# Performance work log

Hardware: AMD Instinct MI355X
Metric: run time of the kernel (lower is better)

## Reference

```python
import jax, jax.numpy as jnp
import numpy as np

N_NODES = 100000
N_EDGES = 800000


def gcn_conv(x, W, b, src, dst, ew, n):
    # PyG GCNConv with edge weights and self-loops already included in (src, dst, ew):
    # deg[i] = sum of incoming edge weights at i; norm_e = d^-1/2[src] * w_e * d^-1/2[dst]
    h = x @ W                                                  # [N, F_out]
    deg = jax.ops.segment_sum(ew, dst, num_segments=n)         # [N]
    dinv = jnp.where(deg > 0, jax.lax.rsqrt(deg), 0.0)
    norm = dinv[src] * ew * dinv[dst]                          # [E]
    out = jax.ops.segment_sum(h[src] * norm[:, None], dst, num_segments=n)
    return out + b


def add_self_loops(edge_index, edge_weight, n):
    loop = jnp.arange(n, dtype=edge_index.dtype)
    src = jnp.concatenate([edge_index[0], loop])
    dst = jnp.concatenate([edge_index[1], loop])
    ew = jnp.concatenate([edge_weight, jnp.ones((n,), edge_weight.dtype)])
    return src, dst, ew


def setup_inputs() -> dict:
    key = jax.random.key(0)
    ks = jax.random.split(key, 10)
    x = jax.random.normal(ks[0], (N_NODES, 5), jnp.float32)
    edge_index = jax.random.randint(ks[1], (2, N_EDGES), 0, N_NODES, dtype=jnp.int64)
    edge_weight = jax.random.uniform(ks[2], (N_EDGES,), jnp.float32)
    def glorot(k, fan_in, fan_out):
        s = float(np.sqrt(6.0 / (fan_in + fan_out)))
        return jax.random.uniform(k, (fan_in, fan_out), jnp.float32, -s, s)
    return {
        "x": x,
        "edge_index": edge_index,
        "edge_weight": edge_weight,
        "W1": glorot(ks[3], 5, 320),
        "b1": jnp.zeros((320,), jnp.float32),
        "W2": glorot(ks[4], 320, 160),
        "b2": jnp.zeros((160,), jnp.float32),
        "We": glorot(ks[5], 160, 80),
        "be": jnp.zeros((80,), jnp.float32),
    }


def reference(x, edge_index, edge_weight, W1, b1, W2, b2, We, be):
    n = x.shape[0]
    src, dst, ew = add_self_loops(edge_index, edge_weight, n)
    h = gcn_conv(x, W1, b1, src, dst, ew, n)        # conv1
    h = jax.nn.relu(h)
    h = gcn_conv(h, W2, b2, src, dst, ew, n)        # conv2
    return h @ We + be                              # embed linear
```

## Files before the change

kernel.cpp:

```cpp
#include <hip/hip_runtime.h>

#define NF0 5
#define F1 320
#define F2 160
#define F3 80
#define NSUB 8
#define SUBCAP 512

typedef float f32x4 __attribute__((ext_vector_type(4)));
typedef _Float16 f16x8 __attribute__((ext_vector_type(8)));


__global__ void k_prep(int padz, int* __restrict__ zreg, int zwords,
                       const float* __restrict__ W2, const float* __restrict__ We,
                       _Float16* __restrict__ Bh,
                       const float* __restrict__ b2, const float* __restrict__ be,
                       float* __restrict__ bc,
                       const unsigned int* __restrict__ ei32, int E, int* __restrict__ flag) {
    __shared__ int ok;
    int b = blockIdx.x;
    if (b < padz) {
        int t = b * 256 + threadIdx.x;
        if (t < zwords) zreg[t] = 0;
        return;
    }
    b -= padz;
    if (b < 13) {
        int t = b * 256 + threadIdx.x;
        if (t >= 50 * 64) return;
        int fid = t >> 6, lane = t & 63;
        int kk = fid / 5, ct = fid % 5;
        int col = ct * 16 + (lane & 15);
        int row0 = kk * 32 + (lane >> 4) * 8;
        float acc[8] = {0.f, 0.f, 0.f, 0.f, 0.f, 0.f, 0.f, 0.f};
        for (int m = 0; m < F2; ++m) {
            float wv = We[m * F3 + col];
            #pragma unroll
            for (int i = 0; i < 8; ++i)
                acc[i] += W2[(size_t)(row0 + i) * F2 + m] * wv;
        }
        size_t ob = (size_t)t * 8;
        #pragma unroll
        for (int i = 0; i < 8; ++i)
            Bh[ob + i] = (_Float16)acc[i];
    } else if (b == 13) {
        int j = threadIdx.x;
        if (j < F3) {
            float s = be[j];
            for (int k = 0; k < F2; ++k) s += b2[k] * We[k * F3 + j];
            bc[j] = s;
        }
    } else {
        if (threadIdx.x == 0) ok = 1;
        __syncthreads();
        int npairs = E < 2048 ? E : 2048;
        for (int i = threadIdx.x; i < npairs; i += blockDim.x)
            if (ei32[2 * i + 1] != 0u) ok = 0;
        __syncthreads();
        if (threadIdx.x == 0) *flag = ok;
    }
}


__global__ void k_binA(const void* ei, const float* __restrict__ ew, const int* __restrict__ flag,
                       int* __restrict__ bin_cnt , int2* __restrict__ bins,
                       int n_bins, int* __restrict__ ovf_n, int* __restrict__ ovf,
                       int ovf_cap, int E) {
    int e = blockIdx.x * blockDim.x + threadIdx.x;
    if (e >= E) return;
    int sub = blockIdx.x & (NSUB - 1);
    int s, d;
    if (*flag) {
        const long long* p = (const long long*)ei;
        s = (int)p[e]; d = (int)p[E + e];
    } else {
        const int* p = (const int*)ei;
        s = p[e]; d = p[E + e];
    }
    float w = ew[e];
    int b = d >> 8;
    int pos = atomicAdd(&bin_cnt[(sub * n_bins + b) * 4], 1);
    if (pos < SUBCAP) {
        int2 pk;
        pk.x = s | ((d & 255) << 24);
        pk.y = __float_as_int(w);
        bins[(size_t)b * (NSUB * SUBCAP) + sub * SUBCAP + pos] = pk;
    } else {
        int o = atomicAdd(ovf_n, 1);
        if (o < ovf_cap) {
            ovf[3 * o] = s; ovf[3 * o + 1] = d; ovf[3 * o + 2] = __float_as_int(w);
        }
    }
}


__global__ __launch_bounds__(512) void k_binB1(const int2* __restrict__ bins,
                                               const int* __restrict__ bin_cnt, int n_bins,
                                               float* __restrict__ dinv,
                                               const int* __restrict__ ovf_n,
                                               const int* __restrict__ ovf, int ovf_cap, int N) {
    __shared__ float deg_l[256];
    int b = blockIdx.x, t = threadIdx.x;
    if (t < 256) deg_l[t] = 0.f;
    __syncthreads();
    int th = t >> 8;
    int tt = t & 255;
    for (int sp = 0; sp < NSUB; sp += 2) {
        int sub = sp + th;
        int ne = bin_cnt[(sub * n_bins + b) * 4]; if (ne > SUBCAP) ne = SUBCAP;
        const int2* bp = bins + (size_t)b * (NSUB * SUBCAP) + sub * SUBCAP;
        for (int j = tt; j < ne; j += 256) {
            int2 pk = bp[j];
            atomicAdd(&deg_l[((unsigned int)pk.x) >> 24], __int_as_float(pk.y));
        }
    }
    int n = *ovf_n; if (n > ovf_cap) n = ovf_cap;
    int lo = b * 256;
    for (int j = t; j < n; j += 512) {
        int d = ovf[3 * j + 1];
        if (d >= lo && d < lo + 256)
            atomicAdd(&deg_l[d - lo], __int_as_float(ovf[3 * j + 2]));
    }
    __syncthreads();
    int node = lo + t;
    if (t < 256 && node < N) dinv[node] = rsqrtf(1.0f + deg_l[t]);
}


__global__ __launch_bounds__(512) void k_binB2(const int2* __restrict__ bins,
                                               const int* __restrict__ bin_cnt, int n_bins,
                                               const float* __restrict__ dinv,
                                               const float* __restrict__ x,
                                               int* __restrict__ cnt, int2* __restrict__ bucket,
                                               int cap, float* __restrict__ agg1,
                                               int* __restrict__ ovf_n, int* __restrict__ ovf,
                                               int ovf_cap, int N) {
    __shared__ int cnt_l[256];
    __shared__ float acc_l[256 * NF0];
    int b = blockIdx.x, t = threadIdx.x;
    if (t < 256) cnt_l[t] = 0;
    for (int q = t; q < 256 * NF0; q += 512) acc_l[q] = 0.f;
    int nsnap = *ovf_n; if (nsnap > ovf_cap) nsnap = ovf_cap;
    __syncthreads();
    int lo = b * 256;

    for (int j = t; j < nsnap; j += 512) {
        int d = ovf[3 * j + 1];
        if (d >= lo && d < lo + 256) {
            int s = ovf[3 * j];
            float w = __int_as_float(ovf[3 * j + 2]) * dinv[s];
            const float* xs = x + (size_t)s * NF0;
            int dl = d - lo;
            #pragma unroll
            for (int f = 0; f < NF0; ++f)
                atomicAdd(&acc_l[dl * NF0 + f], xs[f] * w);
        }
    }

    int th = t >> 8;
    int tt = t & 255;
    for (int sp = 0; sp < NSUB; sp += 2) {
        int sub = sp + th;
        int ne = bin_cnt[(sub * n_bins + b) * 4]; if (ne > SUBCAP) ne = SUBCAP;
        const int2* bp = bins + (size_t)b * (NSUB * SUBCAP) + sub * SUBCAP;
        for (int j = tt; j < ne; j += 256) {
            int2 pk = bp[j];
            int s = pk.x & 0xFFFFFF;
            int dl = ((unsigned int)pk.x) >> 24;
            int node = lo + dl;
            int pos = atomicAdd(&cnt_l[dl], 1);
            if (pos < cap) {
                int2 out_pk; out_pk.x = s; out_pk.y = pk.y;
                bucket[(size_t)node * cap + pos] = out_pk;
            } else {
                int o = atomicAdd(ovf_n, 1);
                if (o < ovf_cap) { ovf[3 * o] = s; ovf[3 * o + 1] = node; ovf[3 * o + 2] = pk.y; }
            }
            float w = __int_as_float(pk.y) * dinv[s];
            const float* xs = x + (size_t)s * NF0;
            float4 sv = *(const float4*)xs;
            float s4 = xs[4];
            atomicAdd(&acc_l[dl * NF0 + 0], sv.x * w);
            atomicAdd(&acc_l[dl * NF0 + 1], sv.y * w);
            atomicAdd(&acc_l[dl * NF0 + 2], sv.z * w);
            atomicAdd(&acc_l[dl * NF0 + 3], sv.w * w);
            atomicAdd(&acc_l[dl * NF0 + 4], s4 * w);
        }
    }
    __syncthreads();

    int node = lo + t;
    if (t < 256 && node < N) {
        float di = dinv[node];
        float sc = di * di;
        const float* xn = x + (size_t)node * NF0;
        float* op = agg1 + (size_t)node * NF0;
        #pragma unroll
        for (int f = 0; f < NF0; ++f)
            op[f] = di * acc_l[t * NF0 + f] + sc * xn[f];
        int c = cnt_l[t]; if (c > cap) c = cap;
        cnt[node] = c;
    }
}


__global__ __launch_bounds__(512) void k_node(const float* __restrict__ agg1,
                                              const float* __restrict__ W1,
                                              const float* __restrict__ b1,
                                              const _Float16* __restrict__ Bh,
                                              const float* __restrict__ dinv,
                                              _Float16* __restrict__ g, int N) {
    __shared__ float W_l[6 * F1];
    __shared__ _Float16 B_l[50 * 64 * 8];
    int tid = threadIdx.x;
    if (tid < 480) {
        float4 v = (tid < 400) ? ((const float4*)W1)[tid] : ((const float4*)b1)[tid - 400];
        ((float4*)W_l)[tid] = v;
    }
    {
        const float4* src = (const float4*)Bh;
        float4* dst = (float4*)B_l;
        for (int i = tid; i < 3200; i += 512) dst[i] = src[i];
    }
    __syncthreads();

    int w = tid >> 6, l = tid & 63;
    int nl = l & 15, kg = l >> 4;
    int base = blockIdx.x * 128 + w * 16;
    int n0 = base + nl;

    float a0v[5] = {0.f, 0.f, 0.f, 0.f, 0.f};
    if (n0 < N) {
        const float* ap = agg1 + (size_t)n0 * NF0;
        #pragma unroll
        for (int j = 0; j < 5; ++j) a0v[j] = ap[j];
    }

    f32x4 zero = {0.f, 0.f, 0.f, 0.f};
    f32x4 acc[5] = {zero, zero, zero, zero, zero};
    const f16x8* blp = (const f16x8*)B_l;

    #pragma unroll
    for (int kk = 0; kk < 10; ++kk) {
        int k0 = kk * 32 + kg * 8;
        float v0[8];
        const float* bb = W_l + 5 * F1 + k0;
        #pragma unroll
        for (int i = 0; i < 8; ++i) v0[i] = bb[i];
        #pragma unroll
        for (int j = 0; j < 5; ++j) {
            const float* wp = W_l + j * F1 + k0;
            float aj0 = a0v[j];
            #pragma unroll
            for (int i = 0; i < 8; ++i) v0[i] += aj0 * wp[i];
        }
        f16x8 ah0, al0;
        #pragma unroll
        for (int i = 0; i < 8; ++i) {
            float t0 = fmaxf(v0[i], 0.f);
            _Float16 h0 = (_Float16)t0;
            ah0[i] = h0;
            al0[i] = (_Float16)(t0 - (float)h0);
        }
        #pragma unroll
        for (int ct = 0; ct < 5; ++ct) {
            f16x8 bf = blp[(kk * 5 + ct) * 64 + l];
            acc[ct] = __builtin_amdgcn_mfma_f32_16x16x32_f16(ah0, bf, acc[ct], 0, 0, 0);
            acc[ct] = __builtin_amdgcn_mfma_f32_16x16x32_f16(al0, bf, acc[ct], 0, 0, 0);
        }
    }

    #pragma unroll
    for (int r = 0; r < 4; ++r) {
        int r0 = base + kg * 4 + r;
        if (r0 < N) {
            float dv = dinv[r0];
            #pragma unroll
            for (int ct = 0; ct < 5; ++ct)
                g[(size_t)r0 * F3 + ct * 16 + nl] = (_Float16)(acc[ct][r] * dv);
        }
    }
}


__global__ __launch_bounds__(256) void k_aggB(const _Float16* __restrict__ g,
                                              const float* __restrict__ dinv,
                                              const float* __restrict__ bc,
                                              const int* __restrict__ cnt,
                                              const int2* __restrict__ bucket, int cap,
                                              float* __restrict__ out, int N) {
    int t = blockIdx.x * blockDim.x + threadIdx.x;
    if (t >= 5 * N) return;
    int i = t / 5;
    int c = (t - i * 5) << 4;
    float acc[16];
    #pragma unroll
    for (int e = 0; e < 16; ++e) acc[e] = 0.f;
    int cn = cnt[i];
    const int4* row4 = (const int4*)(bucket + (size_t)i * cap);
    int j = 0;
    for (; j + 2 <= cn; j += 2) {
        int4 q = row4[j >> 1];
        float w0 = __int_as_float(q.y);
        float w1 = __int_as_float(q.w);
        const f16x8* s0 = (const f16x8*)(g + (size_t)q.x * F3 + c);
        const f16x8* s1 = (const f16x8*)(g + (size_t)q.z * F3 + c);
        f16x8 a0 = s0[0], b0 = s0[1];
        f16x8 a1 = s1[0], b1 = s1[1];
        #pragma unroll
        for (int e = 0; e < 8; ++e) {
            acc[e]     += (float)a0[e] * w0 + (float)a1[e] * w1;
            acc[8 + e] += (float)b0[e] * w0 + (float)b1[e] * w1;
        }
    }
    if (j < cn) {
        int2 p0 = ((const int2*)row4)[j];
        float w0 = __int_as_float(p0.y);
        const f16x8* s0 = (const f16x8*)(g + (size_t)p0.x * F3 + c);
        f16x8 a0 = s0[0], b0 = s0[1];
        #pragma unroll
        for (int e = 0; e < 8; ++e) {
            acc[e]     += (float)a0[e] * w0;
            acc[8 + e] += (float)b0[e] * w0;
        }
    }
    float di = dinv[i];
    const f16x8* sp = (const f16x8*)(g + (size_t)i * F3 + c);
    f16x8 u0 = sp[0], u1 = sp[1];
    const float4* bp = (const float4*)(bc + c);
    float4 q0 = bp[0], q1 = bp[1], q2 = bp[2], q3 = bp[3];
    float4 o0, o1, o2, o3;
    o0.x = di * (acc[0]  + (float)u0[0]) + q0.x;
    o0.y = di * (acc[1]  + (float)u0[1]) + q0.y;
    o0.z = di * (acc[2]  + (float)u0[2]) + q0.z;
    o0.w = di * (acc[3]  + (float)u0[3]) + q0.w;
    o1.x = di * (acc[4]  + (float)u0[4]) + q1.x;
    o1.y = di * (acc[5]  + (float)u0[5]) + q1.y;
    o1.z = di * (acc[6]  + (float)u0[6]) + q1.z;
    o1.w = di * (acc[7]  + (float)u0[7]) + q1.w;
    o2.x = di * (acc[8]  + (float)u1[0]) + q2.x;
    o2.y = di * (acc[9]  + (float)u1[1]) + q2.y;
    o2.z = di * (acc[10] + (float)u1[2]) + q2.z;
    o2.w = di * (acc[11] + (float)u1[3]) + q2.w;
    o3.x = di * (acc[12] + (float)u1[4]) + q3.x;
    o3.y = di * (acc[13] + (float)u1[5]) + q3.y;
    o3.z = di * (acc[14] + (float)u1[6]) + q3.z;
    o3.w = di * (acc[15] + (float)u1[7]) + q3.w;
    float4* op = (float4*)(out + (size_t)i * F3 + c);
    op[0] = o0; op[1] = o1; op[2] = o2; op[3] = o3;
}

__global__ void k_fixB(const _Float16* __restrict__ g, const float* __restrict__ dinv,
                       const int* __restrict__ ovf_n, const int* __restrict__ ovf, int ovf_cap,
                       float* __restrict__ out) {
    int n = *ovf_n; if (n > ovf_cap) n = ovf_cap;
    for (int j = blockIdx.x * blockDim.x + threadIdx.x; j < n; j += gridDim.x * blockDim.x) {
        int s = ovf[3 * j], d = ovf[3 * j + 1];
        float w = dinv[d] * __int_as_float(ovf[3 * j + 2]);
        for (int f = 0; f < F3; ++f)
            atomicAdd(&out[(size_t)d * F3 + f], (float)g[(size_t)s * F3 + f] * w);
    }
}


static inline size_t align256(size_t x) { return (x + 255) & ~(size_t)255; }

extern "C" void kernel_launch(void* const* d_in, const int* in_sizes, int n_in,
                              void* d_out, int out_size, void* d_ws, size_t ws_size,
                              hipStream_t stream) {
    const float* x  = (const float*)d_in[0];
    const void*  ei = d_in[1];
    const float* ew = (const float*)d_in[2];
    const float* W1 = (const float*)d_in[3];
    const float* b1 = (const float*)d_in[4];
    const float* W2 = (const float*)d_in[5];
    const float* b2 = (const float*)d_in[6];
    const float* We = (const float*)d_in[7];
    const float* be = (const float*)d_in[8];
    float* out = (float*)d_out;

    int N = in_sizes[0] / NF0;
    int E = in_sizes[2];

    const int OVF_CAP = 131072;
    int n_bins = (N + 255) >> 8;

    char* p = (char*)d_ws;
    auto alloc = [&](size_t bytes) { char* r = p; p += align256(bytes); return r; };
    int*   flag  = (int*)alloc(4);
    int zwords = 16 + NSUB * n_bins * 4;
    int*   zreg  = (int*)alloc((size_t)zwords * 4);
    int*   ovf_n = zreg;
    int*   bin_cnt = zreg + 16;
    float* dinv  = (float*)alloc((size_t)N * 4);
    int*   cnt   = (int*)  alloc((size_t)N * 4);
    int*   ovf   = (int*)  alloc((size_t)OVF_CAP * 12);
    int2*  bins  = (int2*) alloc((size_t)n_bins * NSUB * SUBCAP * 8);
    float* agg1  = (float*)alloc((size_t)N * NF0 * 4);
    float* bc    = (float*)alloc((size_t)F3 * 4);
    _Float16* Bh = (_Float16*)alloc((size_t)50 * 64 * 8 * 2);
    _Float16* g  = (_Float16*)alloc((size_t)N * F3 * 2);

    size_t used = (size_t)(p - (char*)d_ws);
    int cap = 24;
    if (ws_size > used) {
        size_t avail = (ws_size - used) / ((size_t)N * 8);
        if (avail < (size_t)cap) cap = (int)avail;
    } else cap = 4;
    if (cap < 4) cap = 4;
    int2* bucket = (int2*)alloc((size_t)N * cap * 8);

    int eb   = (E + 255) / 256;
    int padz = (zwords + 255) / 256;

    k_prep<<<padz + 15, 256, 0, stream>>>(padz, zreg, zwords, W2, We, Bh, b2, be, bc,
                                          (const unsigned int*)ei, E, flag);

    k_binA<<<eb, 256, 0, stream>>>(ei, ew, flag, bin_cnt, bins, n_bins, ovf_n, ovf, OVF_CAP, E);
    k_binB1<<<n_bins, 512, 0, stream>>>(bins, bin_cnt, n_bins, dinv, ovf_n, ovf, OVF_CAP, N);
    k_binB2<<<n_bins, 512, 0, stream>>>(bins, bin_cnt, n_bins, dinv, x, cnt, bucket, cap,
                                        agg1, ovf_n, ovf, OVF_CAP, N);

    k_node<<<(N + 127) / 128, 512, 0, stream>>>(agg1, W1, b1, Bh, dinv, g, N);
    k_aggB<<<(5 * N + 255) / 256, 256, 0, stream>>>(g, dinv, bc, cnt, bucket, cap, out, N);
    k_fixB<<<16, 256, 0, stream>>>(g, dinv, ovf_n, ovf, OVF_CAP, out);
}
```

Before: 179.7 us.

## Parallelize weight fold, drop split-fp16 MFMA pass, narrow aggregation threads to 8 features

```diff
diff --git a/kernel.cpp b/kernel.cpp
--- a/kernel.cpp
+++ b/kernel.cpp
@@ -25,25 +25,26 @@
         return;
     }
     b -= padz;
-    if (b < 13) {
+    if (b < 100) {
         int t = b * 256 + threadIdx.x;
-        if (t >= 50 * 64) return;
-        int fid = t >> 6, lane = t & 63;
-        int kk = fid / 5, ct = fid % 5;
-        int col = ct * 16 + (lane & 15);
-        int row0 = kk * 32 + (lane >> 4) * 8;
-        float acc[8] = {0.f, 0.f, 0.f, 0.f, 0.f, 0.f, 0.f, 0.f};
-        for (int m = 0; m < F2; ++m) {
-            float wv = We[m * F3 + col];
-            #pragma unroll
-            for (int i = 0; i < 8; ++i)
-                acc[i] += W2[(size_t)(row0 + i) * F2 + m] * wv;
-        }
-        size_t ob = (size_t)t * 8;
-        #pragma unroll
-        for (int i = 0; i < 8; ++i)
-            Bh[ob + i] = (_Float16)acc[i];
-    } else if (b == 13) {
+        if (t < 25600) {
+            int fid = t >> 9;
+            int rem = t & 511;
+            int lane = rem >> 3, i = rem & 7;
+            int kk = fid / 5, ct = fid - kk * 5;
+            int col = ct * 16 + (lane & 15);
+            int row = kk * 32 + (lane >> 4) * 8 + i;
+            const float* wr = W2 + (size_t)row * F2;
+            float acc = 0.f;
+            #pragma unroll 4
+            for (int m = 0; m < F2; m += 4) {
+                float4 w4 = *(const float4*)(wr + m);
+                acc += w4.x * We[m * F3 + col] + w4.y * We[(m + 1) * F3 + col]
+                     + w4.z * We[(m + 2) * F3 + col] + w4.w * We[(m + 3) * F3 + col];
+            }
+            Bh[((size_t)fid * 64 + lane) * 8 + i] = (_Float16)acc;
+        }
+    } else if (b == 100) {
         int j = threadIdx.x;
         if (j < F3) {
             float s = be[j];
@@ -254,19 +255,14 @@
             #pragma unroll
             for (int i = 0; i < 8; ++i) v0[i] += aj0 * wp[i];
         }
-        f16x8 ah0, al0;
-        #pragma unroll
-        for (int i = 0; i < 8; ++i) {
-            float t0 = fmaxf(v0[i], 0.f);
-            _Float16 h0 = (_Float16)t0;
-            ah0[i] = h0;
-            al0[i] = (_Float16)(t0 - (float)h0);
-        }
+        f16x8 ah0;
+        #pragma unroll
+        for (int i = 0; i < 8; ++i)
+            ah0[i] = (_Float16)fmaxf(v0[i], 0.f);
         #pragma unroll
         for (int ct = 0; ct < 5; ++ct) {
             f16x8 bf = blp[(kk * 5 + ct) * 64 + l];
             acc[ct] = __builtin_amdgcn_mfma_f32_16x16x32_f16(ah0, bf, acc[ct], 0, 0, 0);
-            acc[ct] = __builtin_amdgcn_mfma_f32_16x16x32_f16(al0, bf, acc[ct], 0, 0, 0);
         }
     }
 
@@ -290,12 +286,12 @@
                                               const int2* __restrict__ bucket, int cap,
                                               float* __restrict__ out, int N) {
     int t = blockIdx.x * blockDim.x + threadIdx.x;
-    if (t >= 5 * N) return;
-    int i = t / 5;
-    int c = (t - i * 5) << 4;
-    float acc[16];
+    if (t >= 10 * N) return;
+    int i = t / 10;
+    int c = (t - i * 10) << 3;
+    float acc[8];
     #pragma unroll
-    for (int e = 0; e < 16; ++e) acc[e] = 0.f;
+    for (int e = 0; e < 8; ++e) acc[e] = 0.f;
     int cn = cnt[i];
     const int4* row4 = (const int4*)(bucket + (size_t)i * cap);
     int j = 0;
@@ -303,51 +299,35 @@
         int4 q = row4[j >> 1];
         float w0 = __int_as_float(q.y);
         float w1 = __int_as_float(q.w);
-        const f16x8* s0 = (const f16x8*)(g + (size_t)q.x * F3 + c);
-        const f16x8* s1 = (const f16x8*)(g + (size_t)q.z * F3 + c);
-        f16x8 a0 = s0[0], b0 = s0[1];
-        f16x8 a1 = s1[0], b1 = s1[1];
-        #pragma unroll
-        for (int e = 0; e < 8; ++e) {
-            acc[e]     += (float)a0[e] * w0 + (float)a1[e] * w1;
-            acc[8 + e] += (float)b0[e] * w0 + (float)b1[e] * w1;
-        }
+        f16x8 a0 = *(const f16x8*)(g + (size_t)q.x * F3 + c);
+        f16x8 a1 = *(const f16x8*)(g + (size_t)q.z * F3 + c);
+        #pragma unroll
+        for (int e = 0; e < 8; ++e)
+            acc[e] += (float)a0[e] * w0 + (float)a1[e] * w1;
     }
     if (j < cn) {
         int2 p0 = ((const int2*)row4)[j];
         float w0 = __int_as_float(p0.y);
-        const f16x8* s0 = (const f16x8*)(g + (size_t)p0.x * F3 + c);
-        f16x8 a0 = s0[0], b0 = s0[1];
-        #pragma unroll
-        for (int e = 0; e < 8; ++e) {
-            acc[e]     += (float)a0[e] * w0;
-            acc[8 + e] += (float)b0[e] * w0;
-        }
+        f16x8 a0 = *(const f16x8*)(g + (size_t)p0.x * F3 + c);
+        #pragma unroll
+        for (int e = 0; e < 8; ++e)
+            acc[e] += (float)a0[e] * w0;
     }
     float di = dinv[i];
-    const f16x8* sp = (const f16x8*)(g + (size_t)i * F3 + c);
-    f16x8 u0 = sp[0], u1 = sp[1];
+    f16x8 u0 = *(const f16x8*)(g + (size_t)i * F3 + c);
     const float4* bp = (const float4*)(bc + c);
-    float4 q0 = bp[0], q1 = bp[1], q2 = bp[2], q3 = bp[3];
-    float4 o0, o1, o2, o3;
-    o0.x = di * (acc[0]  + (float)u0[0]) + q0.x;
-    o0.y = di * (acc[1]  + (float)u0[1]) + q0.y;
-    o0.z = di * (acc[2]  + (float)u0[2]) + q0.z;
-    o0.w = di * (acc[3]  + (float)u0[3]) + q0.w;
-    o1.x = di * (acc[4]  + (float)u0[4]) + q1.x;
-    o1.y = di * (acc[5]  + (float)u0[5]) + q1.y;
-    o1.z = di * (acc[6]  + (float)u0[6]) + q1.z;
-    o1.w = di * (acc[7]  + (float)u0[7]) + q1.w;
-    o2.x = di * (acc[8]  + (float)u1[0]) + q2.x;
-    o2.y = di * (acc[9]  + (float)u1[1]) + q2.y;
-    o2.z = di * (acc[10] + (float)u1[2]) + q2.z;
-    o2.w = di * (acc[11] + (float)u1[3]) + q2.w;
-    o3.x = di * (acc[12] + (float)u1[4]) + q3.x;
-    o3.y = di * (acc[13] + (float)u1[5]) + q3.y;
-    o3.z = di * (acc[14] + (float)u1[6]) + q3.z;
-    o3.w = di * (acc[15] + (float)u1[7]) + q3.w;
+    float4 q0 = bp[0], q1 = bp[1];
+    float4 o0, o1;
+    o0.x = di * (acc[0] + (float)u0[0]) + q0.x;
+    o0.y = di * (acc[1] + (float)u0[1]) + q0.y;
+    o0.z = di * (acc[2] + (float)u0[2]) + q0.z;
+    o0.w = di * (acc[3] + (float)u0[3]) + q0.w;
+    o1.x = di * (acc[4] + (float)u0[4]) + q1.x;
+    o1.y = di * (acc[5] + (float)u0[5]) + q1.y;
+    o1.z = di * (acc[6] + (float)u0[6]) + q1.z;
+    o1.w = di * (acc[7] + (float)u0[7]) + q1.w;
     float4* op = (float4*)(out + (size_t)i * F3 + c);
-    op[0] = o0; op[1] = o1; op[2] = o2; op[3] = o3;
+    op[0] = o0; op[1] = o1;
 }
 
 __global__ void k_fixB(const _Float16* __restrict__ g, const float* __restrict__ dinv,
@@ -413,8 +393,8 @@
     int eb   = (E + 255) / 256;
     int padz = (zwords + 255) / 256;
 
-    k_prep<<<padz + 15, 256, 0, stream>>>(padz, zreg, zwords, W2, We, Bh, b2, be, bc,
-                                          (const unsigned int*)ei, E, flag);
+    k_prep<<<padz + 102, 256, 0, stream>>>(padz, zreg, zwords, W2, We, Bh, b2, be, bc,
+                                           (const unsigned int*)ei, E, flag);
 
     k_binA<<<eb, 256, 0, stream>>>(ei, ew, flag, bin_cnt, bins, n_bins, ovf_n, ovf, OVF_CAP, E);
     k_binB1<<<n_bins, 512, 0, stream>>>(bins, bin_cnt, n_bins, dinv, ovf_n, ovf, OVF_CAP, N);
@@ -422,6 +402,6 @@
                                         agg1, ovf_n, ovf, OVF_CAP, N);
 
     k_node<<<(N + 127) / 128, 512, 0, stream>>>(agg1, W1, b1, Bh, dinv, g, N);
-    k_aggB<<<(5 * N + 255) / 256, 256, 0, stream>>>(g, dinv, bc, cnt, bucket, cap, out, N);
+    k_aggB<<<(10 * N + 255) / 256, 256, 0, stream>>>(g, dinv, bc, cnt, bucket, cap, out, N);
     k_fixB<<<16, 256, 0, stream>>>(g, dinv, ovf_n, ovf, OVF_CAP, out);
 }
```

Measured after the change: 156.5 us. -12.9%, faster.
